# Kernel optimization log

Measured on AMD Instinct MI355X. Metric: run time of the kernel, lower is better.

The kernel has to match this reference:

```python
import jax, jax.numpy as jnp
import numpy as np

N, M, D = 256, 64, 1024


def _l2norm(x, axis=-1, eps=1e-12):
    # tf.math.l2_normalize semantics: x / sqrt(max(sum(x^2), eps))
    sq = jnp.sum(x * x, axis=axis, keepdims=True)
    return x * jax.lax.rsqrt(jnp.maximum(sq, eps))


def setup_inputs() -> dict:
    key = jax.random.key(0)
    k1, = jax.random.split(key, 1)
    inputs = jax.random.normal(k1, (N * M, D), dtype=jnp.float32)
    w = jnp.full((1,), 10.0, dtype=jnp.float32)
    b = jnp.full((1,), -5.0, dtype=jnp.float32)
    return {"inputs": inputs, "w": w, "b": b}


def reference(inputs, w, b):
    emb = inputs.reshape(N, M, D)                       # (N, M, D)
    # speaker centroids (normalized mean over utterances)
    center = _l2norm(jnp.mean(emb, axis=1))             # (N, D)
    # leave-one-out centroid per utterance: sum over M minus self (NOT divided)
    center_except = _l2norm(jnp.sum(emb, axis=1, keepdims=True) - emb)  # (N, M, D)
    # off-diagonal similarities: every utterance vs every speaker centroid
    sim_all = jnp.einsum('jmd,id->jmi', emb, center)    # (N_utt_spk j, M, N_centroid i)
    # diagonal (i == j): utterance vs its own leave-one-out centroid
    diag = jnp.sum(center_except * emb, axis=-1)        # (N, M)
    eye = jnp.eye(N, dtype=bool)[:, None, :]            # (N, 1, N)
    sim = jnp.where(eye, diag[:, :, None], sim_all)     # (N, M, N)
    sim = w * sim + b
    return sim.reshape(N * M, N)
```

## Files before the change

kernel.cpp:

```cpp
#include <hip/hip_runtime.h>

#define NSPK 256
#define MUTT 64
#define DDIM 1024
#define NROW (NSPK * MUTT)

using frag_ab = __attribute__((ext_vector_type(8))) short;
using frag_cd = __attribute__((ext_vector_type(4))) float;

static __device__ __forceinline__ unsigned short f32_to_bf16(float f) {
    unsigned int u = __float_as_uint(f);
    return (unsigned short)((u + 0x7FFFu + ((u >> 16) & 1u)) >> 16);
}
static __device__ __forceinline__ unsigned int pack2(float a, float b) {
    return (unsigned)f32_to_bf16(a) | ((unsigned)f32_to_bf16(b) << 16);
}
static __device__ __forceinline__ void gload16(const void* g, void* l) {
    __builtin_amdgcn_global_load_lds(
        (const __attribute__((address_space(1))) unsigned int*)g,
        (__attribute__((address_space(3))) unsigned int*)l, 16, 0, 0);
}


__global__ void __launch_bounds__(256) k_prep(const float* __restrict__ emb,
                                              float* __restrict__ Sp,
                                              unsigned short* __restrict__ ebf,
                                              float* __restrict__ qg) {
    const int j = blockIdx.x;
    const int h = blockIdx.y;
    const int t = threadIdx.x;
    const int lane = t & 63, wave = t >> 6;
    const size_t rowbase = (size_t)j * MUTT + (size_t)h * 16;
    const float* src = emb + rowbase * DDIM + (size_t)t * 4;
    unsigned short* edst = ebf + rowbase * DDIM + (size_t)t * 4;
    __shared__ float qws[16][4];
    float4 s = make_float4(0.f, 0.f, 0.f, 0.f);
    #pragma unroll
    for (int m = 0; m < 16; ++m) {
        float4 v = *(const float4*)(src + (size_t)m * DDIM);
        s.x += v.x; s.y += v.y; s.z += v.z; s.w += v.w;
        float qp = v.x * v.x + v.y * v.y + v.z * v.z + v.w * v.w;
        #pragma unroll
        for (int off = 32; off > 0; off >>= 1) qp += __shfl_down(qp, off, 64);
        if (lane == 0) qws[m][wave] = qp;
        *(uint2*)(edst + (size_t)m * DDIM) = make_uint2(pack2(v.x, v.y), pack2(v.z, v.w));
    }
    __syncthreads();
    if (t < 16) qg[rowbase + t] = qws[t][0] + qws[t][1] + qws[t][2] + qws[t][3];
    *(float4*)(Sp + ((size_t)h * NSPK + j) * DDIM + (size_t)t * 4) = s;
}

template <int P>
__global__ void k_center(const float* __restrict__ Sp, unsigned short* __restrict__ cbf,
                         float* __restrict__ normS2g, float* __restrict__ normSg) {
    const int j = blockIdx.x;
    const int t = threadIdx.x;
    float4 v = make_float4(0.f, 0.f, 0.f, 0.f);
    #pragma unroll
    for (int p = 0; p < P; ++p) {
        float4 a = *(const float4*)(Sp + ((size_t)p * NSPK + j) * DDIM + (size_t)t * 4);
        v.x += a.x; v.y += a.y; v.z += a.z; v.w += a.w;
    }
    float sq = v.x * v.x + v.y * v.y + v.z * v.z + v.w * v.w;
    #pragma unroll
    for (int off = 32; off > 0; off >>= 1) sq += __shfl_down(sq, off, 64);
    __shared__ float ws[4];
    __shared__ float sc_sh;
    const int lane = t & 63, wave = t >> 6;
    if (lane == 0) ws[wave] = sq;
    __syncthreads();
    if (t == 0) {
        float tot = ws[0] + ws[1] + ws[2] + ws[3];
        normS2g[j] = tot;
        normSg[j]  = sqrtf(tot);
        float msq = tot * (1.0f / 4096.0f);
        sc_sh = rsqrtf(fmaxf(msq, 1e-12f)) * (1.0f / 64.0f);
    }
    __syncthreads();
    const float sc = sc_sh;
    *(uint2*)(cbf + (size_t)j * DDIM + (size_t)t * 4) =
        make_uint2(pack2(v.x * sc, v.y * sc), pack2(v.z * sc, v.w * sc));
}

#define BK 64
__global__ void __launch_bounds__(256, 5)
k_gemm4(const unsigned short* __restrict__ ebf, const unsigned short* __restrict__ cbf,
        const float* __restrict__ qg, const float* __restrict__ n2g,
        const float* __restrict__ n1g,
        const float* __restrict__ wp, const float* __restrict__ bp,
        float* __restrict__ out) {
    __shared__ unsigned short lds[2 * 8192];

    const int tid = threadIdx.x, lane = tid & 63, wave = tid >> 6;
    const int rt = blockIdx.x;
    const int ct = blockIdx.y;
    const int row0 = rt * 64;
    const int c0 = ct * 64;
    const int jspk = rt;

    int aoff[2], boff[2];
    #pragma unroll
    for (int i = 0; i < 2; ++i) {
        int c = i * 256 + tid, row = c >> 3, sw = c & 7;
        int off = row * (DDIM * 2) + ((sw ^ (row & 7)) << 4);
        aoff[i] = off; boff[i] = off;
    }
    const int stbase = wave * 512;
    const char* agbase = (const char*)(ebf + (size_t)row0 * DDIM);
    const char* bgbase = (const char*)(cbf + (size_t)c0 * DDIM);

    const int quad = lane >> 4;
    const int m16 = lane & 15;
    const int wrow = wave >> 1, wcol = wave & 1;
    int arow[2], brow[2];
    #pragma unroll
    for (int rr = 0; rr < 2; ++rr) arow[rr] = wrow * 32 + rr * 16 + m16;
    #pragma unroll
    for (int cc = 0; cc < 2; ++cc) brow[cc] = wcol * 32 + cc * 16 + m16;

    frag_cd acc[2][2];
    #pragma unroll
    for (int rr = 0; rr < 2; ++rr)
        #pragma unroll
        for (int cc = 0; cc < 2; ++cc) acc[rr][cc] = (frag_cd){0.f, 0.f, 0.f, 0.f};

    #pragma unroll
    for (int i = 0; i < 2; ++i) {
        gload16(agbase + aoff[i], &lds[i * 2048 + stbase]);
        gload16(bgbase + boff[i], &lds[4096 + i * 2048 + stbase]);
    }
    __syncthreads();

    const int NIT = DDIM / BK;
    for (int it = 0; it < NIT; ++it) {
        const int cur = it & 1;
        if (it + 1 < NIT) {
            const char* ag = agbase + (size_t)(it + 1) * BK * 2;
            const char* bg = bgbase + (size_t)(it + 1) * BK * 2;
            unsigned short* Ln = &lds[(cur ^ 1) * 8192];
            #pragma unroll
            for (int i = 0; i < 2; ++i) {
                gload16(ag + aoff[i], Ln + i * 2048 + stbase);
                gload16(bg + boff[i], Ln + 4096 + i * 2048 + stbase);
            }
        }
        const unsigned short* L = &lds[cur * 8192];
        #pragma unroll
        for (int s = 0; s < 2; ++s) {
            const int kc = (s << 1) + (quad >> 1);
        }
        #pragma unroll
        for (int s = 0; s < 2; ++s) {
            frag_ab af[2], bf[2];
            const int kc = (s << 2) + quad;
            #pragma unroll
            for (int rr = 0; rr < 2; ++rr) {
                int addr = arow[rr] * 128 + ((kc ^ (arow[rr] & 7)) << 4);
                af[rr] = *(const frag_ab*)&L[addr >> 1];
            }
            #pragma unroll
            for (int cc = 0; cc < 2; ++cc) {
                int addr = 8192 + brow[cc] * 128 + ((kc ^ (brow[cc] & 7)) << 4);
                bf[cc] = *(const frag_ab*)&L[addr >> 1];
            }
            #pragma unroll
            for (int rr = 0; rr < 2; ++rr)
                #pragma unroll
                for (int cc = 0; cc < 2; ++cc)
                    acc[rr][cc] = __builtin_amdgcn_mfma_f32_16x16x32_bf16(
                        af[rr], bf[cc], acc[rr][cc], 0, 0, 0);
        }
        __syncthreads();
    }

    const float wv = wp[0], bv = bp[0];
    const float ns2 = n2g[jspk], ns = n1g[jspk];
    #pragma unroll
    for (int rr = 0; rr < 2; ++rr) {
        int rbase = wrow * 32 + rr * 16 + (quad << 2);
        #pragma unroll
        for (int cc = 0; cc < 2; ++cc) {
            int col = c0 + wcol * 32 + cc * 16 + m16;
            frag_cd v = acc[rr][cc];
            #pragma unroll
            for (int r2 = 0; r2 < 4; ++r2) {
                int grow = row0 + rbase + r2;
                float val = v[r2];
                if (col == jspk) {
                    float q = qg[grow];
                    float rd = val * ns;
                    float den2 = ns2 - 2.f * rd + q;
                    val = (rd - q) * rsqrtf(fmaxf(den2, 1e-12f));
                }
                out[(size_t)grow * NSPK + col] = wv * val + bv;
            }
        }
    }
}


__global__ void k_sums(const float* __restrict__ emb, float* __restrict__ Sp) {
    const int j = blockIdx.x;
    const int h = blockIdx.y;
    const int c = threadIdx.x;
    const float* base = emb + ((size_t)j * MUTT + (size_t)h * 32) * DDIM + (size_t)c * 4;
    float4 acc = make_float4(0.f, 0.f, 0.f, 0.f);
    #pragma unroll 8
    for (int m = 0; m < 32; ++m) {
        float4 v = *(const float4*)(base + (size_t)m * DDIM);
        acc.x += v.x; acc.y += v.y; acc.z += v.z; acc.w += v.w;
    }
    *(float4*)(Sp + ((size_t)h * NSPK + j) * DDIM + (size_t)c * 4) = acc;
}

__global__ void __launch_bounds__(256)
k_gemm_old(const float* __restrict__ emb, const unsigned short* __restrict__ cbf,
           const float* __restrict__ normS2g, const float* __restrict__ normSg,
           const float* __restrict__ wp, const float* __restrict__ bp,
           float* __restrict__ out) {
    __shared__ unsigned short Asm[32][32];
    __shared__ unsigned short Bsm[256][32];
    __shared__ float qpart[32][8];
    __shared__ float qfin[32];
    const int tid = threadIdx.x, lane = tid & 63, wave = tid >> 6;
    const int row0 = blockIdx.x * 32;
    const int jspk = row0 >> 6;
    frag_cd acc[2][4];
    #pragma unroll
    for (int rr = 0; rr < 2; ++rr)
        #pragma unroll
        for (int cc = 0; cc < 4; ++cc) acc[rr][cc] = (frag_cd){0.f, 0.f, 0.f, 0.f};
    const int ar = tid >> 3, ak = (tid & 7) << 2;
    const float* aptr = emb + (size_t)(row0 + ar) * DDIM + ak;
    float qacc = 0.f;
    const int bi = tid >> 2, bk = (tid & 3) << 3;
    const int am = lane & 15, kq = (lane >> 4) << 3;
    for (int k0 = 0; k0 < DDIM; k0 += 32) {
        __syncthreads();
        float4 av = *(const float4*)(aptr + k0);
        qacc += av.x * av.x + av.y * av.y + av.z * av.z + av.w * av.w;
        *(uint2*)&Asm[ar][ak] = make_uint2(pack2(av.x, av.y), pack2(av.z, av.w));
        #pragma unroll
        for (int p = 0; p < 4; ++p) {
            int brow = p * 64 + bi;
            *(uint4*)&Bsm[brow][bk] = *(const uint4*)(cbf + (size_t)brow * DDIM + k0 + bk);
        }
        __syncthreads();
        frag_ab afr[2], bfr[4];
        #pragma unroll
        for (int rr = 0; rr < 2; ++rr) afr[rr] = *(const frag_ab*)&Asm[rr * 16 + am][kq];
        #pragma unroll
        for (int cc = 0; cc < 4; ++cc) bfr[cc] = *(const frag_ab*)&Bsm[wave * 64 + cc * 16 + am][kq];
        #pragma unroll
        for (int rr = 0; rr < 2; ++rr)
            #pragma unroll
            for (int cc = 0; cc < 4; ++cc)
                acc[rr][cc] = __builtin_amdgcn_mfma_f32_16x16x32_bf16(afr[rr], bfr[cc], acc[rr][cc], 0, 0, 0);
    }
    qpart[ar][tid & 7] = qacc;
    __syncthreads();
    if (tid < 32) {
        float s = 0.f;
        #pragma unroll
        for (int u = 0; u < 8; ++u) s += qpart[tid][u];
        qfin[tid] = s;
    }
    __syncthreads();
    const float wv = wp[0], bv = bp[0];
    const float ns2 = normS2g[jspk], ns = normSg[jspk];
    #pragma unroll
    for (int rr = 0; rr < 2; ++rr) {
        int rbase = rr * 16 + ((lane >> 4) << 2);
        #pragma unroll
        for (int cc = 0; cc < 4; ++cc) {
            int col = wave * 64 + cc * 16 + (lane & 15);
            frag_cd v = acc[rr][cc];
            #pragma unroll
            for (int r2 = 0; r2 < 4; ++r2) {
                int lrow = rbase + r2;
                float val = v[r2];
                if (col == jspk) {
                    float q = qfin[lrow];
                    float rd = val * ns;
                    float den2 = ns2 - 2.f * rd + q;
                    val = (rd - q) * rsqrtf(fmaxf(den2, 1e-12f));
                }
                out[(size_t)(row0 + lrow) * NSPK + col] = wv * val + bv;
            }
        }
    }
}

extern "C" void kernel_launch(void* const* d_in, const int* in_sizes, int n_in,
                              void* d_out, int out_size, void* d_ws, size_t ws_size,
                              hipStream_t stream) {
    const float* emb = (const float*)d_in[0];
    const float* w   = (const float*)d_in[1];
    const float* b   = (const float*)d_in[2];
    float* out = (float*)d_out;

    const size_t sz_Sp  = (size_t)4 * NSPK * DDIM * 4;
    const size_t sz_ebf = (size_t)NROW * DDIM * 2;
    const size_t sz_cbf = (size_t)NSPK * DDIM * 2;
    const size_t sz_qg  = (size_t)NROW * 4;
    const size_t need = sz_Sp + sz_ebf + sz_cbf + sz_qg + 2 * NSPK * 4;

    if (ws_size >= need) {
        char* p = (char*)d_ws;
        float* Sp = (float*)p;              p += sz_Sp;
        unsigned short* ebf = (unsigned short*)p; p += sz_ebf;
        unsigned short* cbf = (unsigned short*)p; p += sz_cbf;
        float* qg = (float*)p;              p += sz_qg;
        float* n2 = (float*)p;              p += NSPK * 4;
        float* n1 = n2 + NSPK;
        k_prep<<<dim3(NSPK, 4), 256, 0, stream>>>(emb, Sp, ebf, qg);
        k_center<4><<<NSPK, 256, 0, stream>>>(Sp, cbf, n2, n1);
        k_gemm4<<<dim3(NSPK, 4), 256, 0, stream>>>(ebf, cbf, qg, n2, n1, w, b, out);
    } else {
        float* Sp = (float*)d_ws;
        unsigned short* cbf = (unsigned short*)(Sp + 2 * NSPK * DDIM);
        float* n2 = (float*)(cbf + NSPK * DDIM);
        float* n1 = n2 + NSPK;
        k_sums<<<dim3(NSPK, 2), 256, 0, stream>>>(emb, Sp);
        k_center<2><<<NSPK, 256, 0, stream>>>(Sp, cbf, n2, n1);
        k_gemm_old<<<NROW / 32, 256, 0, stream>>>(emb, cbf, n2, n1, w, b, out);
    }
}
```

Baseline: 126.1 us.

## Fuse centroid computation into prep kernel and enlarge GEMM tiles to 128x128

```diff
diff --git a/kernel.cpp b/kernel.cpp
--- a/kernel.cpp
+++ b/kernel.cpp
@@ -22,174 +22,156 @@
 }
 
 
-__global__ void __launch_bounds__(256) k_prep(const float* __restrict__ emb,
-                                              float* __restrict__ Sp,
+__global__ void __launch_bounds__(512) k_prep(const float* __restrict__ emb,
                                               unsigned short* __restrict__ ebf,
-                                              float* __restrict__ qg) {
+                                              unsigned short* __restrict__ cbf,
+                                              float* __restrict__ qg,
+                                              float* __restrict__ n2g,
+                                              float* __restrict__ n1g) {
     const int j = blockIdx.x;
-    const int h = blockIdx.y;
     const int t = threadIdx.x;
+    const int cg = t & 255;
+    const int half = t >> 8;
     const int lane = t & 63, wave = t >> 6;
-    const size_t rowbase = (size_t)j * MUTT + (size_t)h * 16;
-    const float* src = emb + rowbase * DDIM + (size_t)t * 4;
-    unsigned short* edst = ebf + rowbase * DDIM + (size_t)t * 4;
-    __shared__ float qws[16][4];
+    const size_t rb = (size_t)j * MUTT + (size_t)half * 32;
+    const float* src = emb + rb * DDIM + (size_t)cg * 4;
+    unsigned short* edst = ebf + rb * DDIM + (size_t)cg * 4;
+    __shared__ float qws[64][4];
+    __shared__ float4 csum[256];
+    __shared__ float red[4];
+    __shared__ float sc_sh;
     float4 s = make_float4(0.f, 0.f, 0.f, 0.f);
-    #pragma unroll
-    for (int m = 0; m < 16; ++m) {
+    #pragma unroll 8
+    for (int m = 0; m < 32; ++m) {
         float4 v = *(const float4*)(src + (size_t)m * DDIM);
         s.x += v.x; s.y += v.y; s.z += v.z; s.w += v.w;
         float qp = v.x * v.x + v.y * v.y + v.z * v.z + v.w * v.w;
         #pragma unroll
         for (int off = 32; off > 0; off >>= 1) qp += __shfl_down(qp, off, 64);
-        if (lane == 0) qws[m][wave] = qp;
+        if (lane == 0) qws[half * 32 + m][wave & 3] = qp;
         *(uint2*)(edst + (size_t)m * DDIM) = make_uint2(pack2(v.x, v.y), pack2(v.z, v.w));
     }
-    __syncthreads();
-    if (t < 16) qg[rowbase + t] = qws[t][0] + qws[t][1] + qws[t][2] + qws[t][3];
-    *(float4*)(Sp + ((size_t)h * NSPK + j) * DDIM + (size_t)t * 4) = s;
-}
-
-template <int P>
-__global__ void k_center(const float* __restrict__ Sp, unsigned short* __restrict__ cbf,
-                         float* __restrict__ normS2g, float* __restrict__ normSg) {
-    const int j = blockIdx.x;
-    const int t = threadIdx.x;
-    float4 v = make_float4(0.f, 0.f, 0.f, 0.f);
-    #pragma unroll
-    for (int p = 0; p < P; ++p) {
-        float4 a = *(const float4*)(Sp + ((size_t)p * NSPK + j) * DDIM + (size_t)t * 4);
-        v.x += a.x; v.y += a.y; v.z += a.z; v.w += a.w;
-    }
-    float sq = v.x * v.x + v.y * v.y + v.z * v.z + v.w * v.w;
-    #pragma unroll
-    for (int off = 32; off > 0; off >>= 1) sq += __shfl_down(sq, off, 64);
-    __shared__ float ws[4];
-    __shared__ float sc_sh;
-    const int lane = t & 63, wave = t >> 6;
-    if (lane == 0) ws[wave] = sq;
+    if (half) csum[cg] = s;
+    __syncthreads();
+    if (t < 64) qg[(size_t)j * MUTT + t] = qws[t][0] + qws[t][1] + qws[t][2] + qws[t][3];
+    if (!half) {
+        float4 c = csum[cg];
+        s.x += c.x; s.y += c.y; s.z += c.z; s.w += c.w;
+        float sq = s.x * s.x + s.y * s.y + s.z * s.z + s.w * s.w;
+        #pragma unroll
+        for (int off = 32; off > 0; off >>= 1) sq += __shfl_down(sq, off, 64);
+        if (lane == 0) red[wave] = sq;
+    }
     __syncthreads();
     if (t == 0) {
-        float tot = ws[0] + ws[1] + ws[2] + ws[3];
-        normS2g[j] = tot;
-        normSg[j]  = sqrtf(tot);
+        float tot = red[0] + red[1] + red[2] + red[3];
+        n2g[j] = tot;
+        n1g[j] = sqrtf(tot);
         float msq = tot * (1.0f / 4096.0f);
         sc_sh = rsqrtf(fmaxf(msq, 1e-12f)) * (1.0f / 64.0f);
     }
     __syncthreads();
-    const float sc = sc_sh;
-    *(uint2*)(cbf + (size_t)j * DDIM + (size_t)t * 4) =
-        make_uint2(pack2(v.x * sc, v.y * sc), pack2(v.z * sc, v.w * sc));
-}
-
-#define BK 64
-__global__ void __launch_bounds__(256, 5)
-k_gemm4(const unsigned short* __restrict__ ebf, const unsigned short* __restrict__ cbf,
-        const float* __restrict__ qg, const float* __restrict__ n2g,
-        const float* __restrict__ n1g,
-        const float* __restrict__ wp, const float* __restrict__ bp,
-        float* __restrict__ out) {
-    __shared__ unsigned short lds[2 * 8192];
+    if (!half) {
+        const float sc = sc_sh;
+        *(uint2*)(cbf + (size_t)j * DDIM + (size_t)cg * 4) =
+            make_uint2(pack2(s.x * sc, s.y * sc), pack2(s.z * sc, s.w * sc));
+    }
+}
+
+__global__ void __launch_bounds__(256)
+k_gemm(const unsigned short* __restrict__ ebf, const unsigned short* __restrict__ cbf,
+       const float* __restrict__ qg, const float* __restrict__ n2g,
+       const float* __restrict__ n1g,
+       const float* __restrict__ wp, const float* __restrict__ bp,
+       float* __restrict__ out) {
+    __shared__ unsigned short lds[2 * 32768];
 
     const int tid = threadIdx.x, lane = tid & 63, wave = tid >> 6;
     const int rt = blockIdx.x;
     const int ct = blockIdx.y;
-    const int row0 = rt * 64;
-    const int c0 = ct * 64;
-    const int jspk = rt;
-
-    int aoff[2], boff[2];
-    #pragma unroll
-    for (int i = 0; i < 2; ++i) {
-        int c = i * 256 + tid, row = c >> 3, sw = c & 7;
-        int off = row * (DDIM * 2) + ((sw ^ (row & 7)) << 4);
-        aoff[i] = off; boff[i] = off;
-    }
-    const int stbase = wave * 512;
-    const char* agbase = (const char*)(ebf + (size_t)row0 * DDIM);
-    const char* bgbase = (const char*)(cbf + (size_t)c0 * DDIM);
-
-    const int quad = lane >> 4;
-    const int m16 = lane & 15;
+    const int row0 = rt * 128, c0 = ct * 128;
+
+    int goff[8];
+    #pragma unroll
+    for (int i = 0; i < 8; ++i) {
+        int c = i * 256 + tid, row = c >> 4, sw = c & 15;
+        goff[i] = row * (DDIM * 2) + ((sw ^ (row & 15)) << 4);
+    }
+    const int stsh = wave * 512;
+    const char* ag = (const char*)(ebf + (size_t)row0 * DDIM);
+    const char* bg = (const char*)(cbf + (size_t)c0 * DDIM);
+
+    const int quad = lane >> 4, m16 = lane & 15;
     const int wrow = wave >> 1, wcol = wave & 1;
-    int arow[2], brow[2];
-    #pragma unroll
-    for (int rr = 0; rr < 2; ++rr) arow[rr] = wrow * 32 + rr * 16 + m16;
-    #pragma unroll
-    for (int cc = 0; cc < 2; ++cc) brow[cc] = wcol * 32 + cc * 16 + m16;
-
-    frag_cd acc[2][2];
-    #pragma unroll
-    for (int rr = 0; rr < 2; ++rr)
-        #pragma unroll
-        for (int cc = 0; cc < 2; ++cc) acc[rr][cc] = (frag_cd){0.f, 0.f, 0.f, 0.f};
-
-    #pragma unroll
-    for (int i = 0; i < 2; ++i) {
-        gload16(agbase + aoff[i], &lds[i * 2048 + stbase]);
-        gload16(bgbase + boff[i], &lds[4096 + i * 2048 + stbase]);
-    }
-    __syncthreads();
-
-    const int NIT = DDIM / BK;
+
+    frag_cd acc[4][4];
+    #pragma unroll
+    for (int rr = 0; rr < 4; ++rr)
+        #pragma unroll
+        for (int cc = 0; cc < 4; ++cc) acc[rr][cc] = (frag_cd){0.f, 0.f, 0.f, 0.f};
+
+    #pragma unroll
+    for (int i = 0; i < 8; ++i) gload16(ag + goff[i], &lds[i * 2048 + stsh]);
+    #pragma unroll
+    for (int i = 0; i < 8; ++i) gload16(bg + goff[i], &lds[16384 + i * 2048 + stsh]);
+    __syncthreads();
+
+    const int NIT = DDIM / 128;
     for (int it = 0; it < NIT; ++it) {
         const int cur = it & 1;
         if (it + 1 < NIT) {
-            const char* ag = agbase + (size_t)(it + 1) * BK * 2;
-            const char* bg = bgbase + (size_t)(it + 1) * BK * 2;
-            unsigned short* Ln = &lds[(cur ^ 1) * 8192];
-            #pragma unroll
-            for (int i = 0; i < 2; ++i) {
-                gload16(ag + aoff[i], Ln + i * 2048 + stbase);
-                gload16(bg + boff[i], Ln + 4096 + i * 2048 + stbase);
-            }
-        }
-        const unsigned short* L = &lds[cur * 8192];
-        #pragma unroll
-        for (int s = 0; s < 2; ++s) {
-            const int kc = (s << 1) + (quad >> 1);
-        }
-        #pragma unroll
-        for (int s = 0; s < 2; ++s) {
-            frag_ab af[2], bf[2];
+            const char* an = ag + (size_t)(it + 1) * 256;
+            const char* bn = bg + (size_t)(it + 1) * 256;
+            unsigned short* Ln = &lds[(cur ^ 1) * 32768];
+            #pragma unroll
+            for (int i = 0; i < 8; ++i) gload16(an + goff[i], Ln + i * 2048 + stsh);
+            #pragma unroll
+            for (int i = 0; i < 8; ++i) gload16(bn + goff[i], Ln + 16384 + i * 2048 + stsh);
+        }
+        const unsigned short* L = &lds[cur * 32768];
+        #pragma unroll
+        for (int s = 0; s < 4; ++s) {
             const int kc = (s << 2) + quad;
-            #pragma unroll
-            for (int rr = 0; rr < 2; ++rr) {
-                int addr = arow[rr] * 128 + ((kc ^ (arow[rr] & 7)) << 4);
+            frag_ab af[4], bf4[4];
+            #pragma unroll
+            for (int rr = 0; rr < 4; ++rr) {
+                int r = wrow * 64 + rr * 16 + m16;
+                int addr = r * 256 + ((kc ^ (r & 15)) << 4);
                 af[rr] = *(const frag_ab*)&L[addr >> 1];
             }
             #pragma unroll
-            for (int cc = 0; cc < 2; ++cc) {
-                int addr = 8192 + brow[cc] * 128 + ((kc ^ (brow[cc] & 7)) << 4);
-                bf[cc] = *(const frag_ab*)&L[addr >> 1];
+            for (int cc = 0; cc < 4; ++cc) {
+                int r = wcol * 64 + cc * 16 + m16;
+                int addr = 32768 + r * 256 + ((kc ^ (r & 15)) << 4);
+                bf4[cc] = *(const frag_ab*)&L[addr >> 1];
             }
             #pragma unroll
-            for (int rr = 0; rr < 2; ++rr)
+            for (int rr = 0; rr < 4; ++rr)
                 #pragma unroll
-                for (int cc = 0; cc < 2; ++cc)
+                for (int cc = 0; cc < 4; ++cc)
                     acc[rr][cc] = __builtin_amdgcn_mfma_f32_16x16x32_bf16(
-                        af[rr], bf[cc], acc[rr][cc], 0, 0, 0);
+                        af[rr], bf4[cc], acc[rr][cc], 0, 0, 0);
         }
         __syncthreads();
     }
 
     const float wv = wp[0], bv = bp[0];
-    const float ns2 = n2g[jspk], ns = n1g[jspk];
-    #pragma unroll
-    for (int rr = 0; rr < 2; ++rr) {
-        int rbase = wrow * 32 + rr * 16 + (quad << 2);
-        #pragma unroll
-        for (int cc = 0; cc < 2; ++cc) {
-            int col = c0 + wcol * 32 + cc * 16 + m16;
+    #pragma unroll
+    for (int rr = 0; rr < 4; ++rr) {
+        int rbase = wrow * 64 + rr * 16 + (quad << 2);
+        #pragma unroll
+        for (int cc = 0; cc < 4; ++cc) {
+            int col = c0 + wcol * 64 + cc * 16 + m16;
             frag_cd v = acc[rr][cc];
             #pragma unroll
             for (int r2 = 0; r2 < 4; ++r2) {
                 int grow = row0 + rbase + r2;
                 float val = v[r2];
-                if (col == jspk) {
+                int js = grow >> 6;
+                if (col == js) {
                     float q = qg[grow];
-                    float rd = val * ns;
-                    float den2 = ns2 - 2.f * rd + q;
+                    float rd = val * n1g[js];
+                    float den2 = n2g[js] - 2.f * rd + q;
                     val = (rd - q) * rsqrtf(fmaxf(den2, 1e-12f));
                 }
                 out[(size_t)grow * NSPK + col] = wv * val + bv;
@@ -211,6 +193,38 @@
         acc.x += v.x; acc.y += v.y; acc.z += v.z; acc.w += v.w;
     }
     *(float4*)(Sp + ((size_t)h * NSPK + j) * DDIM + (size_t)c * 4) = acc;
+}
+
+template <int P>
+__global__ void k_center(const float* __restrict__ Sp, unsigned short* __restrict__ cbf,
+                         float* __restrict__ normS2g, float* __restrict__ normSg) {
+    const int j = blockIdx.x;
+    const int t = threadIdx.x;
+    float4 v = make_float4(0.f, 0.f, 0.f, 0.f);
+    #pragma unroll
+    for (int p = 0; p < P; ++p) {
+        float4 a = *(const float4*)(Sp + ((size_t)p * NSPK + j) * DDIM + (size_t)t * 4);
+        v.x += a.x; v.y += a.y; v.z += a.z; v.w += a.w;
+    }
+    float sq = v.x * v.x + v.y * v.y + v.z * v.z + v.w * v.w;
+    #pragma unroll
+    for (int off = 32; off > 0; off >>= 1) sq += __shfl_down(sq, off, 64);
+    __shared__ float ws[4];
+    __shared__ float sc_sh;
+    const int lane = t & 63, wave = t >> 6;
+    if (lane == 0) ws[wave] = sq;
+    __syncthreads();
+    if (t == 0) {
+        float tot = ws[0] + ws[1] + ws[2] + ws[3];
+        normS2g[j] = tot;
+        normSg[j]  = sqrtf(tot);
+        float msq = tot * (1.0f / 4096.0f);
+        sc_sh = rsqrtf(fmaxf(msq, 1e-12f)) * (1.0f / 64.0f);
+    }
+    __syncthreads();
+    const float sc = sc_sh;
+    *(uint2*)(cbf + (size_t)j * DDIM + (size_t)t * 4) =
+        make_uint2(pack2(v.x * sc, v.y * sc), pack2(v.z * sc, v.w * sc));
 }
 
 __global__ void __launch_bounds__(256)
@@ -299,23 +313,20 @@
     const float* b   = (const float*)d_in[2];
     float* out = (float*)d_out;
 
-    const size_t sz_Sp  = (size_t)4 * NSPK * DDIM * 4;
     const size_t sz_ebf = (size_t)NROW * DDIM * 2;
     const size_t sz_cbf = (size_t)NSPK * DDIM * 2;
     const size_t sz_qg  = (size_t)NROW * 4;
-    const size_t need = sz_Sp + sz_ebf + sz_cbf + sz_qg + 2 * NSPK * 4;
+    const size_t need = sz_ebf + sz_cbf + sz_qg + 2 * NSPK * 4;
 
     if (ws_size >= need) {
         char* p = (char*)d_ws;
-        float* Sp = (float*)p;              p += sz_Sp;
         unsigned short* ebf = (unsigned short*)p; p += sz_ebf;
         unsigned short* cbf = (unsigned short*)p; p += sz_cbf;
-        float* qg = (float*)p;              p += sz_qg;
-        float* n2 = (float*)p;              p += NSPK * 4;
+        float* qg = (float*)p;                    p += sz_qg;
+        float* n2 = (float*)p;
         float* n1 = n2 + NSPK;
-        k_prep<<<dim3(NSPK, 4), 256, 0, stream>>>(emb, Sp, ebf, qg);
-        k_center<4><<<NSPK, 256, 0, stream>>>(Sp, cbf, n2, n1);
-        k_gemm4<<<dim3(NSPK, 4), 256, 0, stream>>>(ebf, cbf, qg, n2, n1, w, b, out);
+        k_prep<<<NSPK, 512, 0, stream>>>(emb, ebf, cbf, qg, n2, n1);
+        k_gemm<<<dim3(128, 2), 256, 0, stream>>>(ebf, cbf, qg, n2, n1, w, b, out);
     } else {
         float* Sp = (float*)d_ws;
         unsigned short* cbf = (unsigned short*)(Sp + 2 * NSPK * DDIM);
```

New measurement: 135.3 us. +7.3%, slower.

## Use 128x128 GEMM tiles with 32x32 MFMA and two-stage async prefetch

Applied to the files above, without the earlier changes.

```diff
diff --git a/kernel.cpp b/kernel.cpp
--- a/kernel.cpp
+++ b/kernel.cpp
@@ -5,8 +5,9 @@
 #define DDIM 1024
 #define NROW (NSPK * MUTT)
 
-using frag_ab = __attribute__((ext_vector_type(8))) short;
-using frag_cd = __attribute__((ext_vector_type(4))) float;
+using frag_ab  = __attribute__((ext_vector_type(8)))  short;
+using frag_cd  = __attribute__((ext_vector_type(4)))  float;
+using frag_c16 = __attribute__((ext_vector_type(16))) float;
 
 static __device__ __forceinline__ unsigned short f32_to_bf16(float f) {
     unsigned int u = __float_as_uint(f);
@@ -82,114 +83,108 @@
         make_uint2(pack2(v.x * sc, v.y * sc), pack2(v.z * sc, v.w * sc));
 }
 
-#define BK 64
-__global__ void __launch_bounds__(256, 5)
-k_gemm4(const unsigned short* __restrict__ ebf, const unsigned short* __restrict__ cbf,
-        const float* __restrict__ qg, const float* __restrict__ n2g,
-        const float* __restrict__ n1g,
-        const float* __restrict__ wp, const float* __restrict__ bp,
-        float* __restrict__ out) {
-    __shared__ unsigned short lds[2 * 8192];
+__global__ void __launch_bounds__(256)
+k_gemm(const unsigned short* __restrict__ ebf, const unsigned short* __restrict__ cbf,
+       const float* __restrict__ qg, const float* __restrict__ n2g,
+       const float* __restrict__ n1g,
+       const float* __restrict__ wp, const float* __restrict__ bp,
+       float* __restrict__ out) {
+    __shared__ unsigned short lds[2 * 32768];
 
     const int tid = threadIdx.x, lane = tid & 63, wave = tid >> 6;
     const int rt = blockIdx.x;
     const int ct = blockIdx.y;
-    const int row0 = rt * 64;
-    const int c0 = ct * 64;
-    const int jspk = rt;
-
-    int aoff[2], boff[2];
-    #pragma unroll
-    for (int i = 0; i < 2; ++i) {
-        int c = i * 256 + tid, row = c >> 3, sw = c & 7;
-        int off = row * (DDIM * 2) + ((sw ^ (row & 7)) << 4);
-        aoff[i] = off; boff[i] = off;
-    }
-    const int stbase = wave * 512;
-    const char* agbase = (const char*)(ebf + (size_t)row0 * DDIM);
-    const char* bgbase = (const char*)(cbf + (size_t)c0 * DDIM);
-
-    const int quad = lane >> 4;
-    const int m16 = lane & 15;
+    const int row0 = rt * 128, c0 = ct * 128;
+
+    int goff[8];
+    #pragma unroll
+    for (int i = 0; i < 8; ++i) {
+        int c = i * 256 + tid, row = c >> 4, sw = c & 15;
+        goff[i] = row * (DDIM * 2) + ((sw ^ (row & 15)) << 4);
+    }
+    const int stsh = wave * 512;
+    const char* ag = (const char*)(ebf + (size_t)row0 * DDIM);
+    const char* bg = (const char*)(cbf + (size_t)c0 * DDIM);
+
+    const int l31 = lane & 31, l5 = lane >> 5, m16f = lane & 15;
     const int wrow = wave >> 1, wcol = wave & 1;
+
     int arow[2], brow[2];
     #pragma unroll
-    for (int rr = 0; rr < 2; ++rr) arow[rr] = wrow * 32 + rr * 16 + m16;
-    #pragma unroll
-    for (int cc = 0; cc < 2; ++cc) brow[cc] = wcol * 32 + cc * 16 + m16;
-
-    frag_cd acc[2][2];
+    for (int rr = 0; rr < 2; ++rr) arow[rr] = wrow * 64 + rr * 32 + l31;
+    #pragma unroll
+    for (int cc = 0; cc < 2; ++cc) brow[cc] = wcol * 64 + cc * 32 + l31;
+
+    frag_c16 acc[2][2];
     #pragma unroll
     for (int rr = 0; rr < 2; ++rr)
         #pragma unroll
-        for (int cc = 0; cc < 2; ++cc) acc[rr][cc] = (frag_cd){0.f, 0.f, 0.f, 0.f};
-
-    #pragma unroll
-    for (int i = 0; i < 2; ++i) {
-        gload16(agbase + aoff[i], &lds[i * 2048 + stbase]);
-        gload16(bgbase + boff[i], &lds[4096 + i * 2048 + stbase]);
-    }
-    __syncthreads();
-
-    const int NIT = DDIM / BK;
+        for (int cc = 0; cc < 2; ++cc)
+            #pragma unroll
+            for (int q = 0; q < 16; ++q) acc[rr][cc][q] = 0.f;
+
+    auto stage = [&](int buf, int kt) {
+        const char* an = ag + (size_t)kt * 256;
+        const char* bn = bg + (size_t)kt * 256;
+        unsigned short* Ld = &lds[buf * 32768];
+        #pragma unroll
+        for (int i = 0; i < 8; ++i) gload16(an + goff[i], Ld + i * 2048 + stsh);
+        #pragma unroll
+        for (int i = 0; i < 8; ++i) gload16(bn + goff[i], Ld + 16384 + i * 2048 + stsh);
+    };
+
+    stage(0, 0);
+    stage(1, 1);
+
+    const int NIT = DDIM / 128;
+    #pragma unroll
     for (int it = 0; it < NIT; ++it) {
-        const int cur = it & 1;
-        if (it + 1 < NIT) {
-            const char* ag = agbase + (size_t)(it + 1) * BK * 2;
-            const char* bg = bgbase + (size_t)(it + 1) * BK * 2;
-            unsigned short* Ln = &lds[(cur ^ 1) * 8192];
-            #pragma unroll
-            for (int i = 0; i < 2; ++i) {
-                gload16(ag + aoff[i], Ln + i * 2048 + stbase);
-                gload16(bg + boff[i], Ln + 4096 + i * 2048 + stbase);
-            }
-        }
-        const unsigned short* L = &lds[cur * 8192];
-        #pragma unroll
-        for (int s = 0; s < 2; ++s) {
-            const int kc = (s << 1) + (quad >> 1);
-        }
-        #pragma unroll
-        for (int s = 0; s < 2; ++s) {
-            frag_ab af[2], bf[2];
-            const int kc = (s << 2) + quad;
-            #pragma unroll
-            for (int rr = 0; rr < 2; ++rr) {
-                int addr = arow[rr] * 128 + ((kc ^ (arow[rr] & 7)) << 4);
-                af[rr] = *(const frag_ab*)&L[addr >> 1];
-            }
-            #pragma unroll
-            for (int cc = 0; cc < 2; ++cc) {
-                int addr = 8192 + brow[cc] * 128 + ((kc ^ (brow[cc] & 7)) << 4);
-                bf[cc] = *(const frag_ab*)&L[addr >> 1];
-            }
+        if (it < NIT - 1) asm volatile("s_waitcnt vmcnt(16)" ::: "memory");
+        else              asm volatile("s_waitcnt vmcnt(0)"  ::: "memory");
+        __builtin_amdgcn_s_barrier();
+        __builtin_amdgcn_sched_barrier(0);
+
+        const unsigned short* L  = &lds[(it & 1) * 32768];
+        const unsigned short* LB = L + 16384;
+        #pragma unroll
+        for (int ks = 0; ks < 8; ++ks) {
+            const int swb = (((l5 + 2 * ks) & 15) ^ m16f) << 4;
+            frag_ab af[2], bf2[2];
+            #pragma unroll
+            for (int rr = 0; rr < 2; ++rr)
+                af[rr] = *(const frag_ab*)&L[(arow[rr] * 256 + swb) >> 1];
+            #pragma unroll
+            for (int cc = 0; cc < 2; ++cc)
+                bf2[cc] = *(const frag_ab*)&LB[(brow[cc] * 256 + swb) >> 1];
             #pragma unroll
             for (int rr = 0; rr < 2; ++rr)
                 #pragma unroll
                 for (int cc = 0; cc < 2; ++cc)
-                    acc[rr][cc] = __builtin_amdgcn_mfma_f32_16x16x32_bf16(
-                        af[rr], bf[cc], acc[rr][cc], 0, 0, 0);
+                    acc[rr][cc] = __builtin_amdgcn_mfma_f32_32x32x16_bf16(
+                        af[rr], bf2[cc], acc[rr][cc], 0, 0, 0);
         }
-        __syncthreads();
+
+        __builtin_amdgcn_s_barrier();
+        __builtin_amdgcn_sched_barrier(0);
+        if (it + 2 < NIT) stage(it & 1, it + 2);
     }
 
     const float wv = wp[0], bv = bp[0];
-    const float ns2 = n2g[jspk], ns = n1g[jspk];
     #pragma unroll
     for (int rr = 0; rr < 2; ++rr) {
-        int rbase = wrow * 32 + rr * 16 + (quad << 2);
         #pragma unroll
         for (int cc = 0; cc < 2; ++cc) {
-            int col = c0 + wcol * 32 + cc * 16 + m16;
-            frag_cd v = acc[rr][cc];
-            #pragma unroll
-            for (int r2 = 0; r2 < 4; ++r2) {
-                int grow = row0 + rbase + r2;
-                float val = v[r2];
-                if (col == jspk) {
+            frag_c16 v = acc[rr][cc];
+            const int col = c0 + wcol * 64 + cc * 32 + l31;
+            #pragma unroll
+            for (int r = 0; r < 16; ++r) {
+                int grow = row0 + wrow * 64 + rr * 32 + (r & 3) + 8 * (r >> 2) + 4 * l5;
+                float val = v[r];
+                int js = grow >> 6;
+                if (col == js) {
                     float q = qg[grow];
-                    float rd = val * ns;
-                    float den2 = ns2 - 2.f * rd + q;
+                    float rd = val * n1g[js];
+                    float den2 = n2g[js] - 2.f * rd + q;
                     val = (rd - q) * rsqrtf(fmaxf(den2, 1e-12f));
                 }
                 out[(size_t)grow * NSPK + col] = wv * val + bv;
@@ -307,15 +302,15 @@
 
     if (ws_size >= need) {
         char* p = (char*)d_ws;
-        float* Sp = (float*)p;              p += sz_Sp;
+        float* Sp = (float*)p;                    p += sz_Sp;
         unsigned short* ebf = (unsigned short*)p; p += sz_ebf;
         unsigned short* cbf = (unsigned short*)p; p += sz_cbf;
-        float* qg = (float*)p;              p += sz_qg;
-        float* n2 = (float*)p;              p += NSPK * 4;
+        float* qg = (float*)p;                    p += sz_qg;
+        float* n2 = (float*)p;
         float* n1 = n2 + NSPK;
         k_prep<<<dim3(NSPK, 4), 256, 0, stream>>>(emb, Sp, ebf, qg);
         k_center<4><<<NSPK, 256, 0, stream>>>(Sp, cbf, n2, n1);
-        k_gemm4<<<dim3(NSPK, 4), 256, 0, stream>>>(ebf, cbf, qg, n2, n1, w, b, out);
+        k_gemm<<<dim3(128, 2), 256, 0, stream>>>(ebf, cbf, qg, n2, n1, w, b, out);
     } else {
         float* Sp = (float*)d_ws;
         unsigned short* cbf = (unsigned short*)(Sp + 2 * NSPK * DDIM);
```

After: 131.1 us. +3.9%, slower.
